# Kernel tuning notes

Measured on AMD Instinct MI355X. Metric: run time of the kernel, lower is better.

## Reference

```python
import jax, jax.numpy as jnp
import numpy as np

N = 50000          # nodes
E = 400000         # edges
MUL = 32           # multiplicity per irrep
NUM_NEIGHBORS = 8.0
INV_SQRT3 = 1.0 / np.sqrt(3.0)  # w3j(1,1,0) coefficient


def setup_inputs() -> dict:
    key = jax.random.key(0)
    ks = jax.random.split(key, 20)
    inp = {
        # node_input: 32x0e (dim 32) + 32x1o (dim 96) = 128
        "node_input": jax.random.normal(ks[0], (N, 4 * MUL), jnp.float32),
        "node_attr": jnp.ones((N, 1), jnp.float32),           # 1x0e trivial attr
        "edge_src": jax.random.randint(ks[1], (E,), 0, N, jnp.int32),
        "edge_dst": jax.random.randint(ks[2], (E,), 0, N, jnp.int32),
        "edge_attr": jax.random.normal(ks[3], (E, 4), jnp.float32),   # 1x0e + 1x1o
        "edge_scalars": jax.random.normal(ks[4], (E, 16), jnp.float32),
        # FullyConnectedTensorProduct weights (uvw, node_attr has mul 1)
        "w_sc0": jax.random.normal(ks[5], (MUL, MUL), jnp.float32),
        "w_sc1": jax.random.normal(ks[6], (MUL, MUL), jnp.float32),
        "w_lin1_0": jax.random.normal(ks[7], (MUL, MUL), jnp.float32),
        "w_lin1_1": jax.random.normal(ks[8], (MUL, MUL), jnp.float32),
        # radial FC net -> per-edge TP weights (numel = 4*MUL = 128)
        "fc_w1": jax.random.normal(ks[9], (16, 64), jnp.float32),
        "fc_w2": jax.random.normal(ks[10], (64, 4 * MUL), jnp.float32),
        # lin2: irreps_mid (64x0e+64x1o) x attr -> output
        "w_lin2_0": jax.random.normal(ks[11], (2 * MUL, MUL), jnp.float32),
        "w_lin2_1": jax.random.normal(ks[12], (2 * MUL, MUL), jnp.float32),
        # alpha: irreps_mid x attr -> 0e (zero-init in original; small randn for a nontrivial test)
        "w_alpha": 0.1 * jax.random.normal(ks[13], (2 * MUL, 1), jnp.float32),
        # sc_edges: irreps_mid x edge_attr -> edge_attr
        "w_se0a": jax.random.normal(ks[14], (2 * MUL,), jnp.float32),  # mid0e x ea0e -> 0e
        "w_se0b": jax.random.normal(ks[15], (2 * MUL,), jnp.float32),  # mid1o x ea1o -> 0e
        "w_se1a": jax.random.normal(ks[16], (2 * MUL,), jnp.float32),  # mid0e x ea1o -> 1o
        "w_se1b": jax.random.normal(ks[17], (2 * MUL,), jnp.float32),  # mid1o x ea0e -> 1o
    }
    return inp


def reference(node_input, node_attr, edge_src, edge_dst, edge_attr, edge_scalars,
              w_sc0, w_sc1, w_lin1_0, w_lin1_1, fc_w1, fc_w2,
              w_lin2_0, w_lin2_1, w_alpha, w_se0a, w_se0b, w_se1a, w_se1b):
    inv_nn = 1.0 / jnp.sqrt(jnp.asarray(NUM_NEIGHBORS, node_input.dtype))
    n = node_input.shape[0]
    x0 = node_input[:, :MUL]                       # (N, 32)   32x0e
    x1 = node_input[:, MUL:].reshape(n, MUL, 3)    # (N, 32, 3) 32x1o
    a = node_attr                                  # (N, 1)
    s_in = 1.0 / np.sqrt(MUL)                      # FCTP fan-in normalization

    # self-connection: FCTP(input, attr) -> output
    sc0 = (x0 @ w_sc0) * a * s_in
    sc1 = jnp.einsum('num,uw->nwm', x1, w_sc1) * a[:, :, None] * s_in
    node_self = jnp.concatenate([sc0, sc1.reshape(n, 3 * MUL)], axis=1)  # (N, 128)

    # lin1: FCTP(input, attr) -> input irreps
    f0 = (x0 @ w_lin1_0) * a * s_in
    f1 = jnp.einsum('num,uw->nwm', x1, w_lin1_1) * a[:, :, None] * s_in

    # gather source node features per edge
    g0 = f0[edge_src]                              # (E, 32)
    g1 = f1[edge_src]                              # (E, 32, 3)
    ea0 = edge_attr[:, :1]                         # (E, 1)   1x0e
    ea1 = edge_attr[:, 1:]                         # (E, 3)   1x1o

    # radial net -> per-edge TP weights (FullyConnectedNet with sin activation)
    h = jnp.sin(edge_scalars @ fc_w1 * (1.0 / np.sqrt(16.0)))
    w = h @ fc_w2 * (1.0 / np.sqrt(64.0))          # (E, 128)
    wA, wB, wC, wD = jnp.split(w, 4, axis=1)       # each (E, 32)

    # uvu tensor product, 4 instructions
    mA = wA * g0 * ea0                                           # 0e x 0e -> 0e
    mD = wD * jnp.einsum('eum,em->eu', g1, ea1) * INV_SQRT3      # 1o x 1o -> 0e
    mB = (wB * g0)[:, :, None] * ea1[:, None, :]                 # 0e x 1o -> 1o
    mC = (wC[:, :, None] * g1) * ea0[:, :, None]                 # 1o x 0e -> 1o
    mid0 = jnp.concatenate([mA, mD], axis=1)       # (E, 64)  64x0e
    mid1 = jnp.concatenate([mB, mC], axis=1)       # (E, 64, 3) 64x1o

    # scatter-add to destination nodes
    n0 = jax.ops.segment_sum(mid0, edge_dst, num_segments=n) * inv_nn
    n1 = jax.ops.segment_sum(mid1, edge_dst, num_segments=n) * inv_nn

    s_mid = 1.0 / np.sqrt(2 * MUL)
    out0 = (n0 @ w_lin2_0) * a * s_mid
    out1 = jnp.einsum('num,uw->nwm', n1, w_lin2_1) * a[:, :, None] * s_mid
    node_conv = jnp.concatenate([out0, out1.reshape(n, 3 * MUL)], axis=1)

    # alpha gate (sc.output_mask is all ones here, so alpha = 1 - 1 + alpha*1)
    alpha = (n0 @ w_alpha) * a * s_mid             # (N, 1)
    node_conv_out = node_self + alpha * node_conv  # (N, 128)

    # sc_edges: FCTP(mid, edge_attr) -> edge_attr irreps; fan-in = 128 per output
    s_se = 1.0 / np.sqrt(4 * MUL)
    se0 = ((mid0 @ w_se0a) * ea0[:, 0]
           + jnp.einsum('eum,em,u->e', mid1, ea1, w_se0b) * INV_SQRT3) * s_se
    se1 = ((mid0 @ w_se1a)[:, None] * ea1
           + jnp.einsum('eum,u->em', mid1, w_se1b) * ea0) * s_se
    edge_conv_out = edge_attr + jnp.concatenate([se0[:, None], se1], axis=1) * inv_nn

    return node_conv_out, edge_conv_out
```

## Files before the change

kernel.cpp:

```cpp
#include <hip/hip_runtime.h>
#include <math.h>

#define N_NODES 50000
#define E_EDGES 400000
#define NPRE_BLOCKS 6250
#define NHIST_BLOCKS 1563

typedef _Float16 f16x2 __attribute__((ext_vector_type(2)));
typedef _Float16 f16x4 __attribute__((ext_vector_type(4)));
typedef _Float16 f16x8 __attribute__((ext_vector_type(8)));
typedef float    f32x4 __attribute__((ext_vector_type(4)));

static constexpr float S_IN      = 0.17677669529663687f;
static constexpr float S_MID     = 0.125f;
static constexpr float S_SE      = 0.08838834764831843f;
static constexpr float INV_NN    = 0.35355339059327373f;
static constexpr float INV_SQRT3 = 0.5773502691896258f;
static constexpr float FC1_S     = 0.25f;
static constexpr float FC2_S     = 0.125f;

#define BAR_LDS() asm volatile("s_waitcnt lgkmcnt(0)\n\ts_barrier" ::: "memory")

__device__ inline float wave_reduce_dpp(float v) {
    int x;
    x = __builtin_amdgcn_update_dpp(0, __float_as_int(v), 0x111, 0xf, 0xf, true); v += __int_as_float(x);
    x = __builtin_amdgcn_update_dpp(0, __float_as_int(v), 0x112, 0xf, 0xf, true); v += __int_as_float(x);
    x = __builtin_amdgcn_update_dpp(0, __float_as_int(v), 0x114, 0xf, 0xf, true); v += __int_as_float(x);
    x = __builtin_amdgcn_update_dpp(0, __float_as_int(v), 0x118, 0xf, 0xf, true); v += __int_as_float(x);
    x = __builtin_amdgcn_update_dpp(0, __float_as_int(v), 0x142, 0xa, 0xf, true); v += __int_as_float(x);
    x = __builtin_amdgcn_update_dpp(0, __float_as_int(v), 0x143, 0xc, 0xf, true); v += __int_as_float(x);
    return __int_as_float(__builtin_amdgcn_readlane(__float_as_int(v), 63));
}

__global__ __launch_bounds__(256) void pre_hist_kernel(
    const float* __restrict__ node_input, const float* __restrict__ node_attr,
    const float* __restrict__ w_sc0, const float* __restrict__ w_sc1,
    const float* __restrict__ w_lin1_0, const float* __restrict__ w_lin1_1,
    float* __restrict__ out_self, float* __restrict__ ws_f,
    const int* __restrict__ edge_dst, int* __restrict__ counts)
{
    const int t = threadIdx.x;
    if (blockIdx.x >= NPRE_BLOCKS) {
        const int e = (blockIdx.x - NPRE_BLOCKS) * 256 + t;
        if (e < E_EDGES) atomicAdd(&counts[edge_dst[e]], 1);
        return;
    }
    const int n0 = blockIdx.x * 8;
    __shared__ __align__(16) float sx[8 * 128];
    __shared__ float sa[8];
    ((float4*)sx)[t] = ((const float4*)(node_input + (size_t)n0 * 128))[t];
    if (t < 8) sa[t] = node_attr[n0 + t];
    __syncthreads();

    const int half = t >> 7;
    const int idx  = t & 127;
    float wcol[32];
    int m = 0;
    if (idx < 32) {
        const float* __restrict__ W = half ? w_lin1_0 : w_sc0;
        #pragma unroll
        for (int u = 0; u < 32; ++u) wcol[u] = W[u * 32 + idx];
    } else {
        const float* __restrict__ W = half ? w_lin1_1 : w_sc1;
        const int j = idx - 32;
        const int w = j / 3; m = j % 3;
        #pragma unroll
        for (int u = 0; u < 32; ++u) wcol[u] = W[u * 32 + w];
    }
    float* __restrict__ dstp = half ? ws_f : out_self;
    #pragma unroll
    for (int k = 0; k < 8; ++k) {
        const float* x = sx + k * 128;
        float acc = 0.f;
        if (idx < 32) {
            #pragma unroll
            for (int u = 0; u < 32; ++u) acc += x[u] * wcol[u];
        } else {
            #pragma unroll
            for (int u = 0; u < 32; ++u) acc += x[32 + u * 3 + m] * wcol[u];
        }
        dstp[(size_t)(n0 + k) * 128 + idx] = acc * sa[k] * S_IN;
    }
}

__global__ __launch_bounds__(1024) void scan_block_kernel(
    const int* __restrict__ counts, int* __restrict__ cursor, int* __restrict__ bsum)
{
    __shared__ int sd[1024];
    const int t   = threadIdx.x;
    const int idx = blockIdx.x * 1024 + t;
    const int c   = (idx < N_NODES) ? counts[idx] : 0;
    sd[t] = c;
    __syncthreads();
    for (int off = 1; off < 1024; off <<= 1) {
        const int v = (t >= off) ? sd[t - off] : 0;
        __syncthreads();
        sd[t] += v;
        __syncthreads();
    }
    if (idx < N_NODES) cursor[idx] = sd[t] - c;
    if (t == 1023) bsum[blockIdx.x] = sd[1023];
}

__global__ __launch_bounds__(1024) void scan_fixup_kernel(
    int* __restrict__ cursor, const int* __restrict__ bsum)
{
    __shared__ int boff_s;
    const int t = threadIdx.x;
    if (t < 64) {
        int v = (t < (int)blockIdx.x) ? bsum[t] : 0;
        #pragma unroll
        for (int off = 32; off >= 1; off >>= 1) v += __shfl_down(v, off, 64);
        if (t == 0) boff_s = v;
    }
    __syncthreads();
    const int idx = blockIdx.x * 1024 + t;
    if (idx < N_NODES) cursor[idx] += boff_s;
}

__global__ __launch_bounds__(256) void scatter_kernel(
    const int* __restrict__ edge_dst, int* __restrict__ cursor,
    int* __restrict__ sorted_eid)
{
    const int e = blockIdx.x * 256 + threadIdx.x;
    if (e < E_EDGES) {
        const int p = atomicAdd(&cursor[edge_dst[e]], 1);
        sorted_eid[p] = e;
    }
}

__global__ __launch_bounds__(256, 5) void edge_kernel(
    const float* __restrict__ ws_f,
    const int* __restrict__ edge_src, const int* __restrict__ edge_dst,
    const float* __restrict__ edge_attr, const float* __restrict__ edge_scalars,
    const float* __restrict__ fc_w1, const float* __restrict__ fc_w2,
    const float* __restrict__ w_se0a, const float* __restrict__ w_se0b,
    const float* __restrict__ w_se1a, const float* __restrict__ w_se1b,
    const int* __restrict__ sorted_eid,
    float* __restrict__ nacc, float* __restrict__ edge_out)
{
    __shared__ __align__(16) _Float16 sArena[15040];
    __shared__ __align__(16) float sEA[64 * 4];
    __shared__ __align__(16) float sDep[4][36];
    __shared__ int sSRC[64];
    __shared__ int sDST[64];
    __shared__ int sEID[64];

    _Float16* __restrict__ sW2T  = sArena;
    _Float16* __restrict__ sHT   = sArena + 9216;
    _Float16* __restrict__ sWt   = sArena;
    _Float16* __restrict__ sMidA = sArena + 8704;
    _Float16* __restrict__ sBT   = sArena + 12928;

    const int t    = threadIdx.x;
    const int lane = t & 63;
    const int wv   = t >> 6;
    const int quad = lane >> 4;
    const int mm   = lane & 15;
    const int e0   = blockIdx.x * 64;
    const int eb   = wv * 16;

    f16x8 a_w1[4];
    f16x8 b_es = {};
    if (quad < 2) {
        const int myeid = sorted_eid[e0 + eb + mm];
        const float4* esp = (const float4*)edge_scalars + (size_t)myeid * 4 + quad * 2;
        const float4 v0 = esp[0];
        const float4 v1 = esp[1];
        b_es[0] = (_Float16)v0.x; b_es[1] = (_Float16)v0.y;
        b_es[2] = (_Float16)v0.z; b_es[3] = (_Float16)v0.w;
        b_es[4] = (_Float16)v1.x; b_es[5] = (_Float16)v1.y;
        b_es[6] = (_Float16)v1.z; b_es[7] = (_Float16)v1.w;
        const float* wb = fc_w1 + (quad << 3) * 64 + mm;
        #pragma unroll
        for (int jt = 0; jt < 4; ++jt) {
            #pragma unroll
            for (int s = 0; s < 8; ++s)
                a_w1[jt][s] = (_Float16)wb[s * 64 + jt * 16];
        }
    } else {
        #pragma unroll
        for (int jt = 0; jt < 4; ++jt) a_w1[jt] = (f16x8){};
    }

    #pragma unroll
    for (int i = 0; i < 8; ++i) {
        const int u = t + i * 256;
        const int k = u >> 5, c4 = (u & 31) * 4;
        float4 v = ((const float4*)fc_w2)[u];
        sW2T[(c4 + 0) * 72 + k] = (_Float16)v.x;
        sW2T[(c4 + 1) * 72 + k] = (_Float16)v.y;
        sW2T[(c4 + 2) * 72 + k] = (_Float16)v.z;
        sW2T[(c4 + 3) * 72 + k] = (_Float16)v.w;
    }
    if (t < 64) {
        const int eid = sorted_eid[e0 + t];
        *(float4*)&sEA[t * 4] = ((const float4*)edge_attr)[eid];
        sEID[t] = eid;
    } else if (t < 128) {
        sSRC[t - 64] = edge_src[sorted_eid[e0 + (t - 64)]];
    } else if (t < 192) {
        sDST[t - 128] = edge_dst[sorted_eid[e0 + (t - 128)]];
    }
    BAR_LDS();

    const bool hi = lane >= 32;
    const int  u  = lane - 32;
    const int idxA = hi ? (32 + 3 * u) : lane;
    const int idxB = hi ? (33 + 3 * u) : lane;
    const int idxC = hi ? (34 + 3 * u) : lane;
    const int col1 = hi ? (96 + u) : lane;
    const int col2 = hi ? (64 + u) : (32 + lane);

    float ga[4][4], gb[4][4], gc[4][4];
    #pragma unroll
    for (int i = 0; i < 4; ++i) {
        const float* fr = ws_f + (size_t)sSRC[eb + i] * 128;
        ga[0][i] = fr[idxA]; gb[0][i] = fr[idxB]; gc[0][i] = fr[idxC];
    }

    #pragma unroll
    for (int jt = 0; jt < 4; ++jt) {
        f32x4 d = {0.f, 0.f, 0.f, 0.f};
        d = __builtin_amdgcn_mfma_f32_16x16x32_f16(a_w1[jt], b_es, d, 0, 0, 0);
        f16x4 hv;
        hv[0] = (_Float16)__sinf(d[0] * FC1_S);
        hv[1] = (_Float16)__sinf(d[1] * FC1_S);
        hv[2] = (_Float16)__sinf(d[2] * FC1_S);
        hv[3] = (_Float16)__sinf(d[3] * FC1_S);
        *(f16x4*)&sHT[(eb + mm) * 72 + jt * 16 + quad * 4] = hv;
    }
    BAR_LDS();

    f32x4 dacc[8];
    {
        const f16x8 b_lo = *(const f16x8*)&sHT[(eb + mm) * 72 + quad * 8];
        const f16x8 b_hi = *(const f16x8*)&sHT[(eb + mm) * 72 + 32 + quad * 8];
        #pragma unroll
        for (int ct = 0; ct < 8; ++ct) {
            const f16x8 a_lo = *(const f16x8*)&sW2T[(ct * 16 + mm) * 72 + quad * 8];
            const f16x8 a_hi = *(const f16x8*)&sW2T[(ct * 16 + mm) * 72 + 32 + quad * 8];
            f32x4 d = {0.f, 0.f, 0.f, 0.f};
            d = __builtin_amdgcn_mfma_f32_16x16x32_f16(a_lo, b_lo, d, 0, 0, 0);
            d = __builtin_amdgcn_mfma_f32_16x16x32_f16(a_hi, b_hi, d, 0, 0, 0);
            dacc[ct] = d;
        }
    }
    BAR_LDS();

    {
        #pragma unroll
        for (int ct = 0; ct < 8; ++ct) {
            f16x4 v;
            v[0] = (_Float16)(dacc[ct][0] * FC2_S);
            v[1] = (_Float16)(dacc[ct][1] * FC2_S);
            v[2] = (_Float16)(dacc[ct][2] * FC2_S);
            v[3] = (_Float16)(dacc[ct][3] * FC2_S);
            *(f16x4*)&sWt[(eb + mm) * 136 + ct * 16 + quad * 4] = v;
        }
        const f16x8 z8 = {};
        for (int i = t; i < 264; i += 256) *(f16x8*)&sBT[i * 8] = z8;
    }
    BAR_LDS();
    {
        const int uu = t & 63, p = t >> 6;
        const float ev = (p == 0) ? w_se0a[uu] : w_se1b[uu];
        const float ov = (p == 0) ? w_se1a[uu] : w_se0b[uu];
        sBT[(2 * p) * 264 + 4 * uu + p]     = (_Float16)ev;
        sBT[(2 * p + 1) * 264 + 4 * uu + p] = (_Float16)ov;
    }
    BAR_LDS();

    int   cur = -1;
    float am0 = 0.f, axx = 0.f, ayy = 0.f, azz = 0.f;
    _Float16* __restrict__ myA = sMidA + wv * 1056;
    const _Float16* __restrict__ arow = myA + (mm & 3) * 264;
    const _Float16* __restrict__ brow = sBT + (mm & 7) * 264;

    #pragma unroll
    for (int b = 0; b < 4; ++b) {
        if (b < 3) {
            #pragma unroll
            for (int i = 0; i < 4; ++i) {
                const float* fr = ws_f + (size_t)sSRC[eb + (b + 1) * 4 + i] * 128;
                ga[b + 1][i] = fr[idxA]; gb[b + 1][i] = fr[idxB]; gc[b + 1][i] = fr[idxC];
            }
        }
        #pragma unroll
        for (int i = 0; i < 4; ++i) {
            const int el  = eb + b * 4 + i;
            const int dst = sDST[el];
            const float ea0 = sEA[el * 4 + 0];
            const float e1x = sEA[el * 4 + 1];
            const float e1y = sEA[el * 4 + 2];
            const float e1z = sEA[el * 4 + 3];
            const float w1v = (float)sWt[el * 136 + col1];
            const float w2v = (float)sWt[el * 136 + col2];

            float mid0, m1x, m1y, m1z;
            if (!hi) {
                mid0 = w1v * ga[b][i] * ea0;
                const float wbg = w2v * ga[b][i];
                m1x = wbg * e1x; m1y = wbg * e1y; m1z = wbg * e1z;
            } else {
                const float dot = ga[b][i] * e1x + gb[b][i] * e1y + gc[b][i] * e1z;
                mid0 = w1v * dot * INV_SQRT3;
                const float wce = w2v * ea0;
                m1x = wce * ga[b][i]; m1y = wce * gb[b][i]; m1z = wce * gc[b][i];
            }

            if (dst != cur) {
                if (cur >= 0) {
                    float* np_ = nacc + (size_t)cur * 256;
                    atomicAdd(np_ + lane, am0);
                    atomicAdd(np_ + 64 + lane * 3 + 0, axx);
                    atomicAdd(np_ + 64 + lane * 3 + 1, ayy);
                    atomicAdd(np_ + 64 + lane * 3 + 2, azz);
                }
                cur = dst; am0 = axx = ayy = azz = 0.f;
            }
            am0 += mid0; axx += m1x; ayy += m1y; azz += m1z;

            f16x4 mv;
            mv[0] = (_Float16)mid0; mv[1] = (_Float16)m1x;
            mv[2] = (_Float16)m1y;  mv[3] = (_Float16)m1z;
            *(f16x4*)&myA[i * 264 + 4 * lane] = mv;
        }

        f32x4 d = {0.f, 0.f, 0.f, 0.f};
        #pragma unroll
        for (int ks = 0; ks < 8; ++ks) {
            const f16x8 a  = *(const f16x8*)&arow[ks * 32 + quad * 8];
            const f16x8 bb = *(const f16x8*)&brow[ks * 32 + quad * 8];
            d = __builtin_amdgcn_mfma_f32_16x16x32_f16(a, bb, d, 0, 0, 0);
        }
        if (lane < 8) {
            float4 f4; f4.x = d[0]; f4.y = d[1]; f4.z = d[2]; f4.w = d[3];
            *(float4*)&sDep[wv][lane * 4] = f4;
        }
        if (lane < 4) {
            const int el = eb + b * 4 + lane;
            const float c0 = sDep[wv][ 0 + lane], c1 = sDep[wv][ 4 + lane];
            const float c2 = sDep[wv][ 8 + lane], c3 = sDep[wv][12 + lane];
            const float c4 = sDep[wv][16 + lane], c5 = sDep[wv][20 + lane];
            const float c6 = sDep[wv][24 + lane], c7 = sDep[wv][28 + lane];
            const float ea0 = sEA[el * 4 + 0];
            const float e1x = sEA[el * 4 + 1];
            const float e1y = sEA[el * 4 + 2];
            const float e1z = sEA[el * 4 + 3];
            const float s0 = c0 * ea0 + (c3 * e1x + c5 * e1y + c7 * e1z) * INV_SQRT3;
            float4 o;
            o.x = ea0 + s0 * S_SE * INV_NN;
            o.y = e1x + (c1 * e1x + c2 * ea0) * S_SE * INV_NN;
            o.z = e1y + (c1 * e1y + c4 * ea0) * S_SE * INV_NN;
            o.w = e1z + (c1 * e1z + c6 * ea0) * S_SE * INV_NN;
            *(float4*)&edge_out[(size_t)sEID[el] * 4] = o;
        }
    }
    if (cur >= 0) {
        float* np_ = nacc + (size_t)cur * 256;
        atomicAdd(np_ + lane, am0);
        atomicAdd(np_ + 64 + lane * 3 + 0, axx);
        atomicAdd(np_ + 64 + lane * 3 + 1, ayy);
        atomicAdd(np_ + 64 + lane * 3 + 2, azz);
    }
}

__global__ __launch_bounds__(128) void node_post_kernel(
    const float* __restrict__ nacc, const float* __restrict__ node_attr,
    const float* __restrict__ w_lin2_0, const float* __restrict__ w_lin2_1,
    const float* __restrict__ w_alpha, float* __restrict__ out)
{
    const int n0 = blockIdx.x * 8, t = threadIdx.x;
    __shared__ __align__(16) float sn[8 * 256];
    __shared__ float salpha[8];
    const float4* src = (const float4*)(nacc + (size_t)n0 * 256);
    #pragma unroll
    for (int i = 0; i < 4; ++i) ((float4*)sn)[t + i * 128] = src[t + i * 128];
    __syncthreads();

    if (t < 64) {
        const float wa = w_alpha[t];
        #pragma unroll
        for (int k = 0; k < 8; ++k) {
            const float r = wave_reduce_dpp(sn[k * 256 + t] * wa);
            if (t == 0) salpha[k] = r;
        }
    }
    __syncthreads();

    float wcol[64];
    int m = 0;
    if (t < 32) {
        #pragma unroll
        for (int u = 0; u < 64; ++u) wcol[u] = w_lin2_0[u * 32 + t];
    } else {
        const int j = t - 32; const int w = j / 3; m = j % 3;
        #pragma unroll
        for (int u = 0; u < 64; ++u) wcol[u] = w_lin2_1[u * 32 + w];
    }
    #pragma unroll
    for (int k = 0; k < 8; ++k) {
        const float* s = sn + k * 256;
        float acc = 0.f;
        if (t < 32) {
            #pragma unroll
            for (int u = 0; u < 64; ++u) acc += s[u] * wcol[u];
        } else {
            #pragma unroll
            for (int u = 0; u < 64; ++u) acc += s[64 + u * 3 + m] * wcol[u];
        }
        const float a  = node_attr[n0 + k];
        const float sc = a * S_MID * INV_NN;
        const size_t o = (size_t)(n0 + k) * 128 + t;
        out[o] = out[o] + (salpha[k] * sc) * (acc * sc);
    }
}

extern "C" void kernel_launch(void* const* d_in, const int* in_sizes, int n_in,
                              void* d_out, int out_size, void* d_ws, size_t ws_size,
                              hipStream_t stream)
{
    const float* node_input   = (const float*)d_in[0];
    const float* node_attr    = (const float*)d_in[1];
    const int*   edge_src     = (const int*)d_in[2];
    const int*   edge_dst     = (const int*)d_in[3];
    const float* edge_attr    = (const float*)d_in[4];
    const float* edge_scalars = (const float*)d_in[5];
    const float* w_sc0        = (const float*)d_in[6];
    const float* w_sc1        = (const float*)d_in[7];
    const float* w_lin1_0     = (const float*)d_in[8];
    const float* w_lin1_1     = (const float*)d_in[9];
    const float* fc_w1        = (const float*)d_in[10];
    const float* fc_w2        = (const float*)d_in[11];
    const float* w_lin2_0     = (const float*)d_in[12];
    const float* w_lin2_1     = (const float*)d_in[13];
    const float* w_alpha      = (const float*)d_in[14];
    const float* w_se0a       = (const float*)d_in[15];
    const float* w_se0b       = (const float*)d_in[16];
    const float* w_se1a       = (const float*)d_in[17];
    const float* w_se1b       = (const float*)d_in[18];

    float* out      = (float*)d_out;
    float* edge_out = out + (size_t)N_NODES * 128;

    float* ws_f   = (float*)d_ws;
    float* nacc   = ws_f + (size_t)N_NODES * 128;
    int*   counts = (int*)(nacc + (size_t)N_NODES * 256);
    int*   cursor = counts + N_NODES;
    int*   sid    = cursor + N_NODES;
    int*   bsum   = sid + E_EDGES;

    hipMemsetAsync(nacc, 0,
        ((size_t)N_NODES * 256 + N_NODES) * sizeof(float), stream);

    pre_hist_kernel<<<NPRE_BLOCKS + NHIST_BLOCKS, 256, 0, stream>>>(
        node_input, node_attr, w_sc0, w_sc1, w_lin1_0, w_lin1_1, out, ws_f,
        edge_dst, counts);

    scan_block_kernel<<<49, 1024, 0, stream>>>(counts, cursor, bsum);
    scan_fixup_kernel<<<49, 1024, 0, stream>>>(cursor, bsum);
    scatter_kernel<<<(E_EDGES + 255) / 256, 256, 0, stream>>>(edge_dst, cursor, sid);

    edge_kernel<<<E_EDGES / 64, 256, 0, stream>>>(
        ws_f, edge_src, edge_dst, edge_attr, edge_scalars, fc_w1, fc_w2,
        w_se0a, w_se0b, w_se1a, w_se1b, sid, nacc, edge_out);

    node_post_kernel<<<N_NODES / 8, 128, 0, stream>>>(
        nacc, node_attr, w_lin2_0, w_lin2_1, w_alpha, out);
}
```

Before: 420.9 us.

## Store gathered node features and edge scalars in fp16, precompute weight layouts once

Node features for the gather (ws) and edge scalars are now written once in fp16, which halves gather traffic in the edge kernel. Transposed fp16 copies of fc_w2, fc_w1 and the sc_edges B matrix are built once in an extra scan block, so each edge block just copies them instead of converting and transposing per block. The nacc zeroing moves from a large memset into pre_hist, the block scan switches to DPP wave scans, and edge blocks are remapped so each XCD gets a contiguous range. The fp16 storage of the gathered features lowers precision.

```diff
diff --git a/kernel.cpp b/kernel.cpp
--- a/kernel.cpp
+++ b/kernel.cpp
@@ -5,6 +5,7 @@
 #define E_EDGES 400000
 #define NPRE_BLOCKS 6250
 #define NHIST_BLOCKS 1563
+#define NEDGE_BLOCKS 6250
 
 typedef _Float16 f16x2 __attribute__((ext_vector_type(2)));
 typedef _Float16 f16x4 __attribute__((ext_vector_type(4)));
@@ -36,19 +37,36 @@
     const float* __restrict__ node_input, const float* __restrict__ node_attr,
     const float* __restrict__ w_sc0, const float* __restrict__ w_sc1,
     const float* __restrict__ w_lin1_0, const float* __restrict__ w_lin1_1,
-    float* __restrict__ out_self, float* __restrict__ ws_f,
-    const int* __restrict__ edge_dst, int* __restrict__ counts)
+    float* __restrict__ out_self, _Float16* __restrict__ ws_h,
+    const int* __restrict__ edge_dst, int* __restrict__ counts,
+    const float* __restrict__ edge_scalars, _Float16* __restrict__ ES_h,
+    float* __restrict__ nacc)
 {
     const int t = threadIdx.x;
     if (blockIdx.x >= NPRE_BLOCKS) {
         const int e = (blockIdx.x - NPRE_BLOCKS) * 256 + t;
-        if (e < E_EDGES) atomicAdd(&counts[edge_dst[e]], 1);
+        if (e < E_EDGES) {
+            atomicAdd(&counts[edge_dst[e]], 1);
+            const float4* s4 = (const float4*)edge_scalars + (size_t)e * 4;
+            _Float16* dp = ES_h + (size_t)e * 16;
+            #pragma unroll
+            for (int i = 0; i < 4; ++i) {
+                const float4 v = s4[i];
+                f16x4 p = {(_Float16)v.x, (_Float16)v.y, (_Float16)v.z, (_Float16)v.w};
+                *(f16x4*)&dp[i * 4] = p;
+            }
+        }
         return;
     }
     const int n0 = blockIdx.x * 8;
     __shared__ __align__(16) float sx[8 * 128];
     __shared__ float sa[8];
     ((float4*)sx)[t] = ((const float4*)(node_input + (size_t)n0 * 128))[t];
+    {
+        float4* nz = (float4*)(nacc + (size_t)n0 * 256);
+        const float4 z4 = {0.f, 0.f, 0.f, 0.f};
+        nz[t] = z4; nz[t + 256] = z4;
+    }
     if (t < 8) sa[t] = node_attr[n0 + t];
     __syncthreads();
 
@@ -67,7 +85,6 @@
         #pragma unroll
         for (int u = 0; u < 32; ++u) wcol[u] = W[u * 32 + w];
     }
-    float* __restrict__ dstp = half ? ws_f : out_self;
     #pragma unroll
     for (int k = 0; k < 8; ++k) {
         const float* x = sx + k * 128;
@@ -79,27 +96,65 @@
             #pragma unroll
             for (int u = 0; u < 32; ++u) acc += x[32 + u * 3 + m] * wcol[u];
         }
-        dstp[(size_t)(n0 + k) * 128 + idx] = acc * sa[k] * S_IN;
+        const float v = acc * sa[k] * S_IN;
+        if (half) ws_h[(size_t)(n0 + k) * 128 + idx] = (_Float16)v;
+        else      out_self[(size_t)(n0 + k) * 128 + idx] = v;
     }
 }
 
 __global__ __launch_bounds__(1024) void scan_block_kernel(
-    const int* __restrict__ counts, int* __restrict__ cursor, int* __restrict__ bsum)
-{
-    __shared__ int sd[1024];
-    const int t   = threadIdx.x;
+    const int* __restrict__ counts, int* __restrict__ cursor, int* __restrict__ bsum,
+    const float* __restrict__ fc_w1, const float* __restrict__ fc_w2,
+    const float* __restrict__ w_se0a, const float* __restrict__ w_se0b,
+    const float* __restrict__ w_se1a, const float* __restrict__ w_se1b,
+    _Float16* __restrict__ W2T_g, _Float16* __restrict__ W1T_g,
+    _Float16* __restrict__ BT_g)
+{
+    const int t = threadIdx.x;
+    if (blockIdx.x == 49) {
+        for (int u = t; u < 8192; u += 1024) {
+            const int k = u >> 7, c = u & 127;
+            W2T_g[c * 72 + k] = (_Float16)fc_w2[u];
+        }
+        {
+            W2T_g[(t >> 3) * 72 + 64 + (t & 7)] = (_Float16)0.f;
+        }
+        {
+            const int j = t >> 4, k = t & 15;
+            W1T_g[t] = (_Float16)fc_w1[k * 64 + j];
+        }
+        for (int u = t; u < 2112; u += 1024) BT_g[u] = (_Float16)0.f;
+        __syncthreads();
+        if (t < 256) {
+            const int uu = t & 63, p = t >> 6;
+            const float ev = (p == 0) ? w_se0a[uu] : w_se1b[uu];
+            const float ov = (p == 0) ? w_se1a[uu] : w_se0b[uu];
+            BT_g[(2 * p) * 264 + 4 * uu + p]     = (_Float16)ev;
+            BT_g[(2 * p + 1) * 264 + 4 * uu + p] = (_Float16)ov;
+        }
+        return;
+    }
     const int idx = blockIdx.x * 1024 + t;
     const int c   = (idx < N_NODES) ? counts[idx] : 0;
-    sd[t] = c;
+    int v = c, x;
+    x = __builtin_amdgcn_update_dpp(0, v, 0x111, 0xf, 0xf, true); v += x;
+    x = __builtin_amdgcn_update_dpp(0, v, 0x112, 0xf, 0xf, true); v += x;
+    x = __builtin_amdgcn_update_dpp(0, v, 0x114, 0xf, 0xf, true); v += x;
+    x = __builtin_amdgcn_update_dpp(0, v, 0x118, 0xf, 0xf, true); v += x;
+    x = __builtin_amdgcn_update_dpp(0, v, 0x142, 0xa, 0xf, true); v += x;
+    x = __builtin_amdgcn_update_dpp(0, v, 0x143, 0xc, 0xf, true); v += x;
+    __shared__ int swv[16], sex[16];
+    const int wid = t >> 6;
+    if ((t & 63) == 63) swv[wid] = v;
     __syncthreads();
-    for (int off = 1; off < 1024; off <<= 1) {
-        const int v = (t >= off) ? sd[t - off] : 0;
-        __syncthreads();
-        sd[t] += v;
-        __syncthreads();
-    }
-    if (idx < N_NODES) cursor[idx] = sd[t] - c;
-    if (t == 1023) bsum[blockIdx.x] = sd[1023];
+    if (t < 16) {
+        int a = 0;
+        for (int j = 0; j < t; ++j) a += swv[j];
+        sex[t] = a;
+        if (t == 15) bsum[blockIdx.x] = a + swv[15];
+    }
+    __syncthreads();
+    if (idx < N_NODES) cursor[idx] = v - c + sex[wid];
 }
 
 __global__ __launch_bounds__(1024) void scan_fixup_kernel(
@@ -130,12 +185,11 @@
 }
 
 __global__ __launch_bounds__(256, 5) void edge_kernel(
-    const float* __restrict__ ws_f,
+    const _Float16* __restrict__ ws_h,
     const int* __restrict__ edge_src, const int* __restrict__ edge_dst,
-    const float* __restrict__ edge_attr, const float* __restrict__ edge_scalars,
-    const float* __restrict__ fc_w1, const float* __restrict__ fc_w2,
-    const float* __restrict__ w_se0a, const float* __restrict__ w_se0b,
-    const float* __restrict__ w_se1a, const float* __restrict__ w_se1b,
+    const float* __restrict__ edge_attr, const _Float16* __restrict__ ES_h,
+    const _Float16* __restrict__ W2T_g, const _Float16* __restrict__ W1T_g,
+    const _Float16* __restrict__ BT_g,
     const int* __restrict__ sorted_eid,
     float* __restrict__ nacc, float* __restrict__ edge_out)
 {
@@ -157,42 +211,29 @@
     const int wv   = t >> 6;
     const int quad = lane >> 4;
     const int mm   = lane & 15;
-    const int e0   = blockIdx.x * 64;
-    const int eb   = wv * 16;
+
+    const int orig = blockIdx.x;
+    const int xcd  = orig & 7;
+    constexpr int q = NEDGE_BLOCKS >> 3, r = NEDGE_BLOCKS & 7;
+    const int bid = (xcd < r ? xcd * (q + 1) : r * (q + 1) + (xcd - r) * q) + (orig >> 3);
+    const int e0 = bid * 64;
+    const int eb = wv * 16;
 
     f16x8 a_w1[4];
     f16x8 b_es = {};
     if (quad < 2) {
         const int myeid = sorted_eid[e0 + eb + mm];
-        const float4* esp = (const float4*)edge_scalars + (size_t)myeid * 4 + quad * 2;
-        const float4 v0 = esp[0];
-        const float4 v1 = esp[1];
-        b_es[0] = (_Float16)v0.x; b_es[1] = (_Float16)v0.y;
-        b_es[2] = (_Float16)v0.z; b_es[3] = (_Float16)v0.w;
-        b_es[4] = (_Float16)v1.x; b_es[5] = (_Float16)v1.y;
-        b_es[6] = (_Float16)v1.z; b_es[7] = (_Float16)v1.w;
-        const float* wb = fc_w1 + (quad << 3) * 64 + mm;
-        #pragma unroll
-        for (int jt = 0; jt < 4; ++jt) {
-            #pragma unroll
-            for (int s = 0; s < 8; ++s)
-                a_w1[jt][s] = (_Float16)wb[s * 64 + jt * 16];
-        }
+        b_es = *(const f16x8*)&ES_h[(size_t)myeid * 16 + quad * 8];
+        #pragma unroll
+        for (int jt = 0; jt < 4; ++jt)
+            a_w1[jt] = *(const f16x8*)&W1T_g[(jt * 16 + mm) * 16 + quad * 8];
     } else {
         #pragma unroll
         for (int jt = 0; jt < 4; ++jt) a_w1[jt] = (f16x8){};
     }
 
-    #pragma unroll
-    for (int i = 0; i < 8; ++i) {
-        const int u = t + i * 256;
-        const int k = u >> 5, c4 = (u & 31) * 4;
-        float4 v = ((const float4*)fc_w2)[u];
-        sW2T[(c4 + 0) * 72 + k] = (_Float16)v.x;
-        sW2T[(c4 + 1) * 72 + k] = (_Float16)v.y;
-        sW2T[(c4 + 2) * 72 + k] = (_Float16)v.z;
-        sW2T[(c4 + 3) * 72 + k] = (_Float16)v.w;
-    }
+    for (int i = t; i < 1152; i += 256)
+        ((f16x8*)sW2T)[i] = ((const f16x8*)W2T_g)[i];
     if (t < 64) {
         const int eid = sorted_eid[e0 + t];
         *(float4*)&sEA[t * 4] = ((const float4*)edge_attr)[eid];
@@ -215,8 +256,8 @@
     float ga[4][4], gb[4][4], gc[4][4];
     #pragma unroll
     for (int i = 0; i < 4; ++i) {
-        const float* fr = ws_f + (size_t)sSRC[eb + i] * 128;
-        ga[0][i] = fr[idxA]; gb[0][i] = fr[idxB]; gc[0][i] = fr[idxC];
+        const _Float16* fr = ws_h + (size_t)sSRC[eb + i] * 128;
+        ga[0][i] = (float)fr[idxA]; gb[0][i] = (float)fr[idxB]; gc[0][i] = (float)fr[idxC];
     }
 
     #pragma unroll
@@ -258,16 +299,8 @@
             v[3] = (_Float16)(dacc[ct][3] * FC2_S);
             *(f16x4*)&sWt[(eb + mm) * 136 + ct * 16 + quad * 4] = v;
         }
-        const f16x8 z8 = {};
-        for (int i = t; i < 264; i += 256) *(f16x8*)&sBT[i * 8] = z8;
-    }
-    BAR_LDS();
-    {
-        const int uu = t & 63, p = t >> 6;
-        const float ev = (p == 0) ? w_se0a[uu] : w_se1b[uu];
-        const float ov = (p == 0) ? w_se1a[uu] : w_se0b[uu];
-        sBT[(2 * p) * 264 + 4 * uu + p]     = (_Float16)ev;
-        sBT[(2 * p + 1) * 264 + 4 * uu + p] = (_Float16)ov;
+        for (int i = t; i < 264; i += 256)
+            ((f16x8*)sBT)[i] = ((const f16x8*)BT_g)[i];
     }
     BAR_LDS();
 
@@ -282,8 +315,10 @@
         if (b < 3) {
             #pragma unroll
             for (int i = 0; i < 4; ++i) {
-                const float* fr = ws_f + (size_t)sSRC[eb + (b + 1) * 4 + i] * 128;
-                ga[b + 1][i] = fr[idxA]; gb[b + 1][i] = fr[idxB]; gc[b + 1][i] = fr[idxC];
+                const _Float16* fr = ws_h + (size_t)sSRC[eb + (b + 1) * 4 + i] * 128;
+                ga[b + 1][i] = (float)fr[idxA];
+                gb[b + 1][i] = (float)fr[idxB];
+                gc[b + 1][i] = (float)fr[idxC];
             }
         }
         #pragma unroll
@@ -444,27 +479,31 @@
     float* out      = (float*)d_out;
     float* edge_out = out + (size_t)N_NODES * 128;
 
-    float* ws_f   = (float*)d_ws;
-    float* nacc   = ws_f + (size_t)N_NODES * 128;
+    _Float16* ws_h = (_Float16*)d_ws;
+    _Float16* ES_h = ws_h + (size_t)N_NODES * 128;
+    float* nacc   = (float*)((char*)d_ws + (size_t)N_NODES * 128 * 4);
     int*   counts = (int*)(nacc + (size_t)N_NODES * 256);
     int*   cursor = counts + N_NODES;
     int*   sid    = cursor + N_NODES;
     int*   bsum   = sid + E_EDGES;
-
-    hipMemsetAsync(nacc, 0,
-        ((size_t)N_NODES * 256 + N_NODES) * sizeof(float), stream);
+    _Float16* W2T_g = (_Float16*)(bsum + 64);
+    _Float16* W1T_g = W2T_g + 9216;
+    _Float16* BT_g  = W1T_g + 1024;
+
+    hipMemsetAsync(counts, 0, N_NODES * sizeof(int), stream);
 
     pre_hist_kernel<<<NPRE_BLOCKS + NHIST_BLOCKS, 256, 0, stream>>>(
-        node_input, node_attr, w_sc0, w_sc1, w_lin1_0, w_lin1_1, out, ws_f,
-        edge_dst, counts);
-
-    scan_block_kernel<<<49, 1024, 0, stream>>>(counts, cursor, bsum);
+        node_input, node_attr, w_sc0, w_sc1, w_lin1_0, w_lin1_1, out, ws_h,
+        edge_dst, counts, edge_scalars, ES_h, nacc);
+
+    scan_block_kernel<<<50, 1024, 0, stream>>>(counts, cursor, bsum,
+        fc_w1, fc_w2, w_se0a, w_se0b, w_se1a, w_se1b, W2T_g, W1T_g, BT_g);
     scan_fixup_kernel<<<49, 1024, 0, stream>>>(cursor, bsum);
     scatter_kernel<<<(E_EDGES + 255) / 256, 256, 0, stream>>>(edge_dst, cursor, sid);
 
-    edge_kernel<<<E_EDGES / 64, 256, 0, stream>>>(
-        ws_f, edge_src, edge_dst, edge_attr, edge_scalars, fc_w1, fc_w2,
-        w_se0a, w_se0b, w_se1a, w_se1b, sid, nacc, edge_out);
+    edge_kernel<<<NEDGE_BLOCKS, 256, 0, stream>>>(
+        ws_h, edge_src, edge_dst, edge_attr, ES_h, W2T_g, W1T_g, BT_g,
+        sid, nacc, edge_out);
 
     node_post_kernel<<<N_NODES / 8, 128, 0, stream>>>(
         nacc, node_attr, w_lin2_0, w_lin2_1, w_alpha, out);
```

Measured after the change: 416.8 us. Within noise of the previous version (-1.0%).
